# Kernel optimization log

Measured on AMD Instinct MI355X. Metric: run time of the kernel, lower is better.

Reference implementation:

```python
import jax, jax.numpy as jnp
import numpy as np

# NVFP4 e2m1 representable magnitudes and nearest-rounding decision boundaries
FP4_GRID = jnp.array([0.0, 0.5, 1.0, 1.5, 2.0, 3.0, 4.0, 6.0], dtype=jnp.float32)
FP4_BOUNDS = jnp.array([0.25, 0.75, 1.25, 1.75, 2.5, 3.5, 5.0], dtype=jnp.float32)
E4M3_MAX = 448.0
FP4_MAX = 6.0
BLOCK = 16  # NVFP4 block size along K


def round_fp4(x):
    """Round to nearest FP4 (e2m1) representable value (saturating at +-6)."""
    idx = jnp.searchsorted(FP4_BOUNDS, jnp.abs(x))
    return jnp.sign(x) * FP4_GRID[idx]


def cast_e4m3(x):
    """Saturating cast through float8_e4m3fn and back to fp32."""
    return jnp.clip(x, -E4M3_MAX, E4M3_MAX).astype(jnp.float8_e4m3fn).astype(jnp.float32)


def setup_inputs() -> dict:
    key = jax.random.key(0)
    kx, kw, kb = jax.random.split(key, 3)
    M, N, K = 32, 8192, 8192
    x = jax.random.normal(kx, (M, K), dtype=jnp.float32)
    w = jax.random.normal(kw, (N, K), dtype=jnp.float32)
    bias = jax.random.normal(kb, (N,), dtype=jnp.float32)

    # raw global scales: amax / (448 * 6)  (== 1 / fp4_global_scale)
    weight_scale_2 = jnp.max(jnp.abs(w)) / (E4M3_MAX * FP4_MAX)
    input_scale = jnp.max(jnp.abs(x)) / (E4M3_MAX * FP4_MAX)

    # offline NVFP4 quantization of the weight (as done in __init__)
    wb = w.reshape(N, K // BLOCK, BLOCK)
    sf = jnp.max(jnp.abs(wb), axis=-1) / FP4_MAX              # [N, K//16] per-block scale
    weight_scale = cast_e4m3(sf / weight_scale_2)             # fp8 block scales (values)
    dscale = weight_scale[..., None] * weight_scale_2         # per-element dequant scale
    safe = jnp.where(dscale > 0, dscale, 1.0)
    w_fp4 = jnp.where(dscale > 0, round_fp4(wb / safe), 0.0).reshape(N, K)

    return {
        "x": x,
        "weight_fp4": w_fp4,
        "bias": bias,
        "input_scale": input_scale.reshape(1),
        "weight_scale": weight_scale,
        "weight_scale_2": weight_scale_2.reshape(1),
    }


def reference(x, weight_fp4, bias, input_scale, weight_scale, weight_scale_2):
    N, K = weight_fp4.shape
    M = x.shape[0]
    # --- weight dequant: fp4 value * fp8 block scale * global scale ---
    w_dq = (weight_fp4.reshape(N, K // BLOCK, BLOCK)
            * weight_scale[..., None] * weight_scale_2).reshape(N, K)
    # --- dynamic NVFP4 fake-quant of the activation ---
    xb = x.reshape(M, K // BLOCK, BLOCK)
    sf = cast_e4m3(jnp.max(jnp.abs(xb), axis=-1) / FP4_MAX / input_scale)  # [M, K//16]
    scale = sf[..., None] * input_scale                                    # per-element scale
    safe = jnp.where(scale > 0, scale, 1.0)
    x_dq = jnp.where(scale > 0, round_fp4(xb / safe) * scale, 0.0).reshape(M, K)
    # --- linear ---
    return x_dq @ w_dq.T + bias
```

## Files before the change

### kernel.cpp

```cpp
#include <hip/hip_runtime.h>

typedef float f32x4 __attribute__((ext_vector_type(4)));
typedef short s16x8 __attribute__((ext_vector_type(8)));

#define M_DIM 32
#define N_DIM 8192
#define K_DIM 8192
#define NBLK (K_DIM / 16)

__device__ inline unsigned short f2bf(float f) {
    unsigned int u = __float_as_uint(f);
    u = (u + 0x7FFFu + ((u >> 16) & 1u)) >> 16;
    return (unsigned short)u;
}

__device__ inline float round_fp4(float x) {
    float a = fabsf(x);
    float g;
    if (a > 2.5f)        g = (a > 5.0f) ? 6.0f : ((a > 3.5f) ? 4.0f : 3.0f);
    else if (a > 1.25f)  g = (a > 1.75f) ? 2.0f : 1.5f;
    else                 g = (a > 0.75f) ? 1.0f : ((a > 0.25f) ? 0.5f : 0.0f);
    return copysignf(g, x);
}

__device__ inline float cast_e4m3(float v) {
    v = fminf(v, 448.0f);
    if (v < 0.015625f) {
        return rintf(v * 512.0f) * (1.0f / 512.0f);
    }
    int e; float m = frexpf(v, &e);
    return ldexpf(rintf(m * 16.0f) * 0.0625f, e);
}

__global__ void quant_pack_x(const float* __restrict__ x,
                             const float* __restrict__ input_scale,
                             unsigned short* __restrict__ xpack) {
    int tid = blockIdx.x * blockDim.x + threadIdx.x;
    int m = tid >> 9;
    int b = tid & 511;
    const float is = input_scale[0];

    const float* xp = x + (size_t)m * K_DIM + b * 16;
    f32x4 l0 = *(const f32x4*)(xp);
    f32x4 l1 = *(const f32x4*)(xp + 4);
    f32x4 l2 = *(const f32x4*)(xp + 8);
    f32x4 l3 = *(const f32x4*)(xp + 12);
    float v[16];
    #pragma unroll
    for (int i = 0; i < 4; ++i) { v[i]=l0[i]; v[4+i]=l1[i]; v[8+i]=l2[i]; v[12+i]=l3[i]; }

    float amax = 0.f;
    #pragma unroll
    for (int i = 0; i < 16; ++i) amax = fmaxf(amax, fabsf(v[i]));

    float sf = cast_e4m3(amax / 6.0f / is);
    float scale = sf * is;

    int kstep = b >> 1;
    int t = m >> 4;
    int mrow = m & 15;
    unsigned short* base = xpack + (size_t)kstep * 64 * 16;
    #pragma unroll
    for (int i = 0; i < 16; ++i) {
        float q = 0.f;
        if (scale > 0.f) q = round_fp4(v[i] / scale) * scale;
        int g = ((b & 1) << 1) + (i >> 3);
        int lane = g * 16 + mrow;
        int j = i & 7;
        base[(size_t)lane * 16 + t * 8 + j] = f2bf(q);
    }
}

__global__ __launch_bounds__(512) void gemm_kernel(
    const float* __restrict__ W,
    const float* __restrict__ wscale,
    const float* __restrict__ ws2p,
    const float* __restrict__ bias,
    const unsigned short* __restrict__ xpack,
    float* __restrict__ out)
{
    __shared__ float red[8][512];
    const int wave = threadIdx.x >> 6;
    const int lane = threadIdx.x & 63;
    const int lrow = lane & 15;
    const int lgrp = lane >> 4;
    const int n0 = blockIdx.x * 16;
    const int n = n0 + lrow;
    const float ws2 = ws2p[0];

    const int k_begin = wave * (K_DIM / 8);
    const int ksteps = (K_DIM / 8) / 32;

    const float* wrow = W + (size_t)n * K_DIM + k_begin + lgrp * 8;
    const float* srow = wscale + (size_t)n * NBLK + (k_begin >> 4) + (lgrp >> 1);
    const unsigned short* xp = xpack + ((size_t)(k_begin >> 5) * 64 + lane) * 16;

    f32x4 acc0 = {0.f, 0.f, 0.f, 0.f};
    f32x4 acc1 = {0.f, 0.f, 0.f, 0.f};

    #pragma unroll 4
    for (int s = 0; s < ksteps; ++s) {
        f32x4 a0 = *(const f32x4*)(wrow);
        f32x4 a1 = *(const f32x4*)(wrow + 4);
        float sc = srow[2 * s] * ws2;
        s16x8 b0 = *(const s16x8*)(xp);
        s16x8 b1 = *(const s16x8*)(xp + 8);
        s16x8 af;
        #pragma unroll
        for (int j = 0; j < 4; ++j) af[j]     = (short)f2bf(a0[j] * sc);
        #pragma unroll
        for (int j = 0; j < 4; ++j) af[4 + j] = (short)f2bf(a1[j] * sc);
        acc0 = __builtin_amdgcn_mfma_f32_16x16x32_bf16(af, b0, acc0, 0, 0, 0);
        acc1 = __builtin_amdgcn_mfma_f32_16x16x32_bf16(af, b1, acc1, 0, 0, 0);
        wrow += 32;
        xp += 64 * 16;
    }

    float* my = red[wave];
    #pragma unroll
    for (int r = 0; r < 4; ++r) {
        my[lane * 8 + r]     = acc0[r];
        my[lane * 8 + 4 + r] = acc1[r];
    }
    __syncthreads();

    int i = threadIdx.x;
    float vsum = 0.f;
    #pragma unroll
    for (int w = 0; w < 8; ++w) vsum += red[w][i];
    int l = i >> 3, t = (i >> 2) & 1, r = i & 3;
    int nn = n0 + ((l >> 4) << 2) + r;
    int mm = t * 16 + (l & 15);
    out[(size_t)mm * N_DIM + nn] = vsum + bias[nn];
}

extern "C" void kernel_launch(void* const* d_in, const int* in_sizes, int n_in,
                              void* d_out, int out_size, void* d_ws, size_t ws_size,
                              hipStream_t stream) {
    const float* x           = (const float*)d_in[0];
    const float* weight_fp4  = (const float*)d_in[1];
    const float* bias        = (const float*)d_in[2];
    const float* input_scale = (const float*)d_in[3];
    const float* wscale      = (const float*)d_in[4];
    const float* ws2         = (const float*)d_in[5];
    float* out = (float*)d_out;
    unsigned short* xpack = (unsigned short*)d_ws;

    quant_pack_x<<<64, 256, 0, stream>>>(x, input_scale, xpack);
    gemm_kernel<<<512, 512, 0, stream>>>(weight_fp4, wscale, ws2, bias, xpack, out);
}
```

Baseline: 83.10 us.

## Stage GEMM operands through LDS with async global-to-LDS double buffering

```diff
diff --git a/kernel.cpp b/kernel.cpp
--- a/kernel.cpp
+++ b/kernel.cpp
@@ -7,6 +7,11 @@
 #define N_DIM 8192
 #define K_DIM 8192
 #define NBLK (K_DIM / 16)
+#define KSTEPS 32
+#define DEPTH 2
+#define OPS 5
+#define SLOT_BYTES 4352
+#define WAVE_LDS (DEPTH * SLOT_BYTES)
 
 __device__ inline unsigned short f2bf(float f) {
     unsigned int u = __float_as_uint(f);
@@ -32,6 +37,23 @@
     return ldexpf(rintf(m * 16.0f) * 0.0625f, e);
 }
 
+__device__ __forceinline__ void async_copy16(const void* g, void* l) {
+    __builtin_amdgcn_global_load_lds((const __attribute__((address_space(1))) void*)g,
+                                     (__attribute__((address_space(3))) void*)l, 16, 0, 0);
+}
+__device__ __forceinline__ void async_copy4(const void* g, void* l) {
+    __builtin_amdgcn_global_load_lds((const __attribute__((address_space(1))) void*)g,
+                                     (__attribute__((address_space(3))) void*)l, 4, 0, 0);
+}
+
+template <int VM>
+__device__ __forceinline__ void waitvm() {
+    asm volatile("s_waitcnt vmcnt(%0)" :: "i"(VM) : "memory");
+}
+__device__ __forceinline__ void wait_lds_reads_done() {
+    asm volatile("s_waitcnt lgkmcnt(0)" ::: "memory");
+}
+
 __global__ void quant_pack_x(const float* __restrict__ x,
                              const float* __restrict__ input_scale,
                              unsigned short* __restrict__ xpack) {
@@ -71,7 +93,7 @@
     }
 }
 
-__global__ __launch_bounds__(512) void gemm_kernel(
+__global__ __launch_bounds__(512, 4) void gemm_kernel(
     const float* __restrict__ W,
     const float* __restrict__ wscale,
     const float* __restrict__ ws2p,
@@ -79,7 +101,8 @@
     const unsigned short* __restrict__ xpack,
     float* __restrict__ out)
 {
-    __shared__ float red[8][512];
+    __shared__ __align__(16) unsigned char lds[8 * WAVE_LDS];
+
     const int wave = threadIdx.x >> 6;
     const int lane = threadIdx.x & 63;
     const int lrow = lane & 15;
@@ -89,22 +112,37 @@
     const float ws2 = ws2p[0];
 
     const int k_begin = wave * (K_DIM / 8);
-    const int ksteps = (K_DIM / 8) / 32;
-
-    const float* wrow = W + (size_t)n * K_DIM + k_begin + lgrp * 8;
-    const float* srow = wscale + (size_t)n * NBLK + (k_begin >> 4) + (lgrp >> 1);
-    const unsigned short* xp = xpack + ((size_t)(k_begin >> 5) * 64 + lane) * 16;
+
+    const float* wsrc = W + (size_t)n * K_DIM + k_begin + lgrp * 8;
+    const unsigned short* xsrc =
+        xpack + ((size_t)(k_begin >> 5) * 64 + lane) * 16;
+    const float* ssrc = wscale + (size_t)n * NBLK + (k_begin >> 4) + (lgrp >> 1);
+
+    unsigned char* wb = lds + wave * WAVE_LDS;
 
     f32x4 acc0 = {0.f, 0.f, 0.f, 0.f};
     f32x4 acc1 = {0.f, 0.f, 0.f, 0.f};
 
-    #pragma unroll 4
-    for (int s = 0; s < ksteps; ++s) {
-        f32x4 a0 = *(const f32x4*)(wrow);
-        f32x4 a1 = *(const f32x4*)(wrow + 4);
-        float sc = srow[2 * s] * ws2;
-        s16x8 b0 = *(const s16x8*)(xp);
-        s16x8 b1 = *(const s16x8*)(xp + 8);
+    auto stage = [&](int s) {
+        unsigned char* sb = wb + (s & (DEPTH - 1)) * SLOT_BYTES;
+        const float* wp = wsrc + s * 32;
+        async_copy16(wp,     sb +    0);
+        async_copy16(wp + 4, sb + 1024);
+        const unsigned short* xq = xsrc + s * 1024;
+        async_copy16(xq,     sb + 2048);
+        async_copy16(xq + 8, sb + 3072);
+        async_copy4(ssrc + 2 * s, sb + 4096);
+    };
+
+    auto step = [&](int s, bool do_stage) {
+        const unsigned char* sb = wb + (s & (DEPTH - 1)) * SLOT_BYTES;
+        f32x4 a0 = *(const f32x4*)(sb +    0 + lane * 16);
+        f32x4 a1 = *(const f32x4*)(sb + 1024 + lane * 16);
+        s16x8 b0 = *(const s16x8*)(sb + 2048 + lane * 16);
+        s16x8 b1 = *(const s16x8*)(sb + 3072 + lane * 16);
+        float sc = *(const float*)(sb + 4096 + lane * 4) * ws2;
+        wait_lds_reads_done();
+        if (do_stage) stage(s + DEPTH);
         s16x8 af;
         #pragma unroll
         for (int j = 0; j < 4; ++j) af[j]     = (short)f2bf(a0[j] * sc);
@@ -112,11 +150,22 @@
         for (int j = 0; j < 4; ++j) af[4 + j] = (short)f2bf(a1[j] * sc);
         acc0 = __builtin_amdgcn_mfma_f32_16x16x32_bf16(af, b0, acc0, 0, 0, 0);
         acc1 = __builtin_amdgcn_mfma_f32_16x16x32_bf16(af, b1, acc1, 0, 0, 0);
-        wrow += 32;
-        xp += 64 * 16;
-    }
-
-    float* my = red[wave];
+    };
+
+    stage(0);
+    stage(1);
+
+    #pragma unroll 2
+    for (int s = 0; s < KSTEPS - DEPTH; ++s) {
+        waitvm<OPS>();
+        step(s, true);
+    }
+    waitvm<OPS>(); step(KSTEPS - 2, false);
+    waitvm<0>();   step(KSTEPS - 1, false);
+
+    __syncthreads();
+    float* red = (float*)lds;
+    float* my = red + wave * 512;
     #pragma unroll
     for (int r = 0; r < 4; ++r) {
         my[lane * 8 + r]     = acc0[r];
@@ -127,7 +176,7 @@
     int i = threadIdx.x;
     float vsum = 0.f;
     #pragma unroll
-    for (int w = 0; w < 8; ++w) vsum += red[w][i];
+    for (int w = 0; w < 8; ++w) vsum += red[w * 512 + i];
     int l = i >> 3, t = (i >> 2) & 1, r = i & 3;
     int nn = n0 + ((l >> 4) << 2) + r;
     int mm = t * 16 + (l & 15);
```

Result: slower. 87.58 us (+5.4%).

## Split K across blocks with atomic reduction, prefetch loads, stage scales in LDS

Applied to the files above, without the earlier changes.

```diff
diff --git a/kernel.cpp b/kernel.cpp
--- a/kernel.cpp
+++ b/kernel.cpp
@@ -7,6 +7,9 @@
 #define N_DIM 8192
 #define K_DIM 8192
 #define NBLK (K_DIM / 16)
+#define KSPLIT 4
+#define WSTEPS 16
+#define SCL_LD 129
 
 __device__ inline unsigned short f2bf(float f) {
     unsigned int u = __float_as_uint(f);
@@ -30,6 +33,12 @@
     }
     int e; float m = frexpf(v, &e);
     return ldexpf(rintf(m * 16.0f) * 0.0625f, e);
+}
+
+__global__ void init_out(const float* __restrict__ bias, float* __restrict__ out) {
+    int i = blockIdx.x * blockDim.x + threadIdx.x;
+    f32x4 b = *(const f32x4*)(bias + ((i * 4) & (N_DIM - 1)));
+    *(f32x4*)(out + (size_t)i * 4) = b;
 }
 
 __global__ void quant_pack_x(const float* __restrict__ x,
@@ -59,7 +68,7 @@
     int kstep = b >> 1;
     int t = m >> 4;
     int mrow = m & 15;
-    unsigned short* base = xpack + (size_t)kstep * 64 * 16;
+    unsigned short* base = xpack + (size_t)kstep * 1024 + t * 512;
     #pragma unroll
     for (int i = 0; i < 16; ++i) {
         float q = 0.f;
@@ -67,71 +76,91 @@
         int g = ((b & 1) << 1) + (i >> 3);
         int lane = g * 16 + mrow;
         int j = i & 7;
-        base[(size_t)lane * 16 + t * 8 + j] = f2bf(q);
+        base[lane * 8 + j] = f2bf(q);
     }
 }
 
-__global__ __launch_bounds__(512) void gemm_kernel(
+__global__ __launch_bounds__(256, 8) void gemm_kernel(
     const float* __restrict__ W,
     const float* __restrict__ wscale,
     const float* __restrict__ ws2p,
-    const float* __restrict__ bias,
     const unsigned short* __restrict__ xpack,
     float* __restrict__ out)
 {
-    __shared__ float red[8][512];
+    __shared__ float shm[16 * SCL_LD];
+
     const int wave = threadIdx.x >> 6;
     const int lane = threadIdx.x & 63;
     const int lrow = lane & 15;
     const int lgrp = lane >> 4;
     const int n0 = blockIdx.x * 16;
-    const int n = n0 + lrow;
+    const int kb = blockIdx.y;
     const float ws2 = ws2p[0];
 
-    const int k_begin = wave * (K_DIM / 8);
-    const int ksteps = (K_DIM / 8) / 32;
-
-    const float* wrow = W + (size_t)n * K_DIM + k_begin + lgrp * 8;
-    const float* srow = wscale + (size_t)n * NBLK + (k_begin >> 4) + (lgrp >> 1);
-    const unsigned short* xp = xpack + ((size_t)(k_begin >> 5) * 64 + lane) * 16;
-
-    f32x4 acc0 = {0.f, 0.f, 0.f, 0.f};
-    f32x4 acc1 = {0.f, 0.f, 0.f, 0.f};
-
-    #pragma unroll 4
-    for (int s = 0; s < ksteps; ++s) {
-        f32x4 a0 = *(const f32x4*)(wrow);
-        f32x4 a1 = *(const f32x4*)(wrow + 4);
-        float sc = srow[2 * s] * ws2;
-        s16x8 b0 = *(const s16x8*)(xp);
-        s16x8 b1 = *(const s16x8*)(xp + 8);
-        s16x8 af;
+    {
+        int t = threadIdx.x;
+        int row = t >> 4;
+        int c0 = (t & 15) * 8;
+        const float* s = wscale + (size_t)(n0 + row) * NBLK + kb * 128 + c0;
         #pragma unroll
-        for (int j = 0; j < 4; ++j) af[j]     = (short)f2bf(a0[j] * sc);
-        #pragma unroll
-        for (int j = 0; j < 4; ++j) af[4 + j] = (short)f2bf(a1[j] * sc);
-        acc0 = __builtin_amdgcn_mfma_f32_16x16x32_bf16(af, b0, acc0, 0, 0, 0);
-        acc1 = __builtin_amdgcn_mfma_f32_16x16x32_bf16(af, b1, acc1, 0, 0, 0);
-        wrow += 32;
-        xp += 64 * 16;
-    }
-
-    float* my = red[wave];
-    #pragma unroll
-    for (int r = 0; r < 4; ++r) {
-        my[lane * 8 + r]     = acc0[r];
-        my[lane * 8 + 4 + r] = acc1[r];
+        for (int j = 0; j < 8; ++j)
+            shm[row * SCL_LD + c0 + j] = s[j] * ws2;
     }
     __syncthreads();
 
-    int i = threadIdx.x;
-    float vsum = 0.f;
+    const int kofs = kb * 2048 + wave * 512;
+    const float* wcur = W + (size_t)(n0 + lrow) * K_DIM + kofs + lgrp * 8;
+    const unsigned short* xcur = xpack + (size_t)(kofs >> 5) * 1024 + lane * 8;
+    const float* sbase = shm + lrow * SCL_LD + wave * 32 + (lgrp >> 1);
+
+    f32x4 acc0 = {0,0,0,0}, acc1 = {0,0,0,0};
+
+    f32x4 a0 = *(const f32x4*)(wcur);
+    f32x4 a1 = *(const f32x4*)(wcur + 4);
+    s16x8 b0 = *(const s16x8*)(xcur);
+    s16x8 b1 = *(const s16x8*)(xcur + 512);
+
     #pragma unroll
-    for (int w = 0; w < 8; ++w) vsum += red[w][i];
-    int l = i >> 3, t = (i >> 2) & 1, r = i & 3;
-    int nn = n0 + ((l >> 4) << 2) + r;
-    int mm = t * 16 + (l & 15);
-    out[(size_t)mm * N_DIM + nn] = vsum + bias[nn];
+    for (int s = 0; s < WSTEPS; ++s) {
+        f32x4 na0, na1; s16x8 nb0, nb1;
+        if (s + 1 < WSTEPS) {
+            na0 = *(const f32x4*)(wcur + 32);
+            na1 = *(const f32x4*)(wcur + 36);
+            nb0 = *(const s16x8*)(xcur + 1024);
+            nb1 = *(const s16x8*)(xcur + 1536);
+        }
+        float sc = sbase[s * 2];
+        s16x8 af;
+        #pragma unroll
+        for (int j = 0; j < 4; ++j) {
+            af[j]     = (short)f2bf(a0[j] * sc);
+            af[4 + j] = (short)f2bf(a1[j] * sc);
+        }
+        acc0 = __builtin_amdgcn_mfma_f32_16x16x32_bf16(af, b0, acc0, 0, 0, 0);
+        acc1 = __builtin_amdgcn_mfma_f32_16x16x32_bf16(af, b1, acc1, 0, 0, 0);
+        a0 = na0; a1 = na1; b0 = nb0; b1 = nb1;
+        wcur += 32;
+        xcur += 1024;
+    }
+
+    __syncthreads();
+    float* red = shm;
+    #pragma unroll
+    for (int r = 0; r < 4; ++r) {
+        red[wave * 512 + lane * 8 + r]     = acc0[r];
+        red[wave * 512 + lane * 8 + 4 + r] = acc1[r];
+    }
+    __syncthreads();
+
+    #pragma unroll
+    for (int h = 0; h < 2; ++h) {
+        int j = threadIdx.x + h * 256;
+        float v = red[j] + red[512 + j] + red[1024 + j] + red[1536 + j];
+        int l = j >> 3, t = (j >> 2) & 1, r = j & 3;
+        int m = t * 16 + (l & 15);
+        int n = n0 + ((l >> 4) << 2) + r;
+        atomicAdd(out + (size_t)m * N_DIM + n, v);
+    }
 }
 
 extern "C" void kernel_launch(void* const* d_in, const int* in_sizes, int n_in,
@@ -146,6 +175,7 @@
     float* out = (float*)d_out;
     unsigned short* xpack = (unsigned short*)d_ws;
 
+    init_out<<<256, 256, 0, stream>>>(bias, out);
     quant_pack_x<<<64, 256, 0, stream>>>(x, input_scale, xpack);
-    gemm_kernel<<<512, 512, 0, stream>>>(weight_fp4, wscale, ws2, bias, xpack, out);
+    gemm_kernel<<<dim3(512, KSPLIT), 256, 0, stream>>>(weight_fp4, wscale, ws2, xpack, out);
 }
```

After: 73.72 us. 1.13x faster.
